# Performance work log

Hardware: AMD Instinct MI355X
Metric: run time of the kernel (lower is better)

## Reference

```python
import jax, jax.numpy as jnp
import numpy as np

B, L, D = 2, 2048, 1024
H, HD = 16, 64

def setup_inputs() -> dict:
    key = jax.random.key(0)
    ks = jax.random.split(key, 5)
    x = jax.random.normal(ks[0], (B, L, D), dtype=jnp.float32)
    mask = jnp.ones((B, L, L), dtype=bool)
    # torch nn.Linear weights: [out_features, in_features]
    s = 1.0 / np.sqrt(D)
    wq = jax.random.normal(ks[1], (H * HD, D), dtype=jnp.float32) * s
    wk = jax.random.normal(ks[2], (H * HD, D), dtype=jnp.float32) * s
    wv = jax.random.normal(ks[3], (H * HD, D), dtype=jnp.float32) * s
    wo = jax.random.normal(ks[4], (D, H * HD), dtype=jnp.float32) * s
    return {"x": x, "mask": mask, "wq": wq, "wk": wk, "wv": wv, "wo": wo}

def reference(x, mask, wq, wk, wv, wo):
    b, l, d = x.shape
    scale = jnp.sqrt(jnp.float32(HD))
    # projections (Linear: x @ W.T), then split heads -> [B,H,L,HD]
    q = (x @ wq.T).reshape(b, l, H, HD).transpose(0, 2, 1, 3)
    k = (x @ wk.T).reshape(b, l, H, HD).transpose(0, 2, 1, 3)
    v = (x @ wv.T).reshape(b, l, H, HD).transpose(0, 2, 1, 3)
    scores = jnp.einsum('bhqd,bhkd->bhqk', q, k) / scale
    scores = jnp.where(mask[:, None, :, :], scores, -jnp.inf)
    attn = jax.nn.softmax(scores, axis=-1)
    out = jnp.einsum('bhqk,bhkd->bhqd', attn, v)
    out = out.transpose(0, 2, 1, 3).reshape(b, l, H * HD)
    return out @ wo.T
```

## Files before the change

kernel.cpp:

```cpp
#include <hip/hip_runtime.h>
#include <hip/hip_bf16.h>

#define B_ 2
#define L_ 2048
#define D_ 1024
#define H_ 16
#define HD_ 64

typedef __bf16 bf16_t;
typedef bf16_t bf16x8 __attribute__((ext_vector_type(8)));
typedef bf16_t bf16x4 __attribute__((ext_vector_type(4)));
typedef float f32x2 __attribute__((ext_vector_type(2)));
typedef float f32x4 __attribute__((ext_vector_type(4)));
typedef float f32x16 __attribute__((ext_vector_type(16)));
typedef unsigned int u32x4 __attribute__((ext_vector_type(4)));

static __device__ __forceinline__ f32x4 mfma16(bf16x8 a, bf16x8 b, f32x4 c) {
    return __builtin_amdgcn_mfma_f32_16x16x32_bf16(a, b, c, 0, 0, 0);
}
static __device__ __forceinline__ f32x16 mfma32(bf16x8 a, bf16x8 b, f32x16 c) {
    return __builtin_amdgcn_mfma_f32_32x32x16_bf16(a, b, c, 0, 0, 0);
}
static __device__ __forceinline__ unsigned cvtpk(float a, float b) {
    unsigned r;
    asm("v_cvt_pk_bf16_f32 %0, %1, %2" : "=v"(r) : "v"(a), "v"(b));
    return r;
}

__global__ void cvt_all(const float* __restrict__ x,  const float* __restrict__ wq,
                        const float* __restrict__ wk, const float* __restrict__ wv,
                        const float* __restrict__ wo, bf16_t* __restrict__ dst) {
    const int NX = B_ * L_ * D_;
    const int NW = D_ * D_;
    int i = (blockIdx.x * blockDim.x + threadIdx.x) * 4;
    const float* s; int off;
    if      (i < NX)          { s = x;  off = i; }
    else if (i < NX + NW)     { s = wq; off = i - NX; }
    else if (i < NX + 2 * NW) { s = wk; off = i - NX - NW; }
    else if (i < NX + 3 * NW) { s = wv; off = i - NX - 2 * NW; }
    else                      { s = wo; off = i - NX - 3 * NW; }
    float4 v = *reinterpret_cast<const float4*>(s + off);
    bf16x4 o;
    o[0] = (bf16_t)v.x; o[1] = (bf16_t)v.y; o[2] = (bf16_t)v.z; o[3] = (bf16_t)v.w;
    *reinterpret_cast<bf16x4*>(dst + i) = o;
}

template<int MODE>
__global__ __launch_bounds__(256) void gemm_lds(const bf16_t* __restrict__ A,
                                                const bf16_t* __restrict__ Bt,
                                                void* __restrict__ Cout) {
    constexpr int K = 1024;
    __shared__ __align__(16) bf16_t lA[2][128][32];
    __shared__ __align__(16) bf16_t lB[2][128][32];
    const int tid = threadIdx.x, wave = tid >> 6, lane = tid & 63;
    const int lo = lane & 15, hi = lane >> 4;
    const int bm = blockIdx.x * 128, bn = blockIdx.y * 128;
    const int wm = (wave >> 1) * 64, wn = (wave & 1) * 64;
    const int srow = wave * 32 + (lane >> 2);
    const int skel = (lane & 3) * 8;

    const bf16_t* Abase = A  + (size_t)(bm + srow) * K + skel;
    const bf16_t* Bbase = Bt + (size_t)(bn + srow) * K + skel;

    auto stage = [&](int buf, int k0) {
#pragma unroll
        for (int t = 0; t < 2; ++t) {
            __builtin_amdgcn_global_load_lds(
                (const __attribute__((address_space(1))) void*)(Abase + (size_t)t * 16 * K + k0),
                (__attribute__((address_space(3))) void*)&lA[buf][wave * 32 + t * 16][0],
                16, 0, 0);
            __builtin_amdgcn_global_load_lds(
                (const __attribute__((address_space(1))) void*)(Bbase + (size_t)t * 16 * K + k0),
                (__attribute__((address_space(3))) void*)&lB[buf][wave * 32 + t * 16][0],
                16, 0, 0);
        }
    };

    f32x4 acc[4][4] = {};
    auto compute = [&](int buf) {
        bf16x8 af[4], bfr[4];
#pragma unroll
        for (int i = 0; i < 4; ++i)
            af[i] = *reinterpret_cast<const bf16x8*>(&lA[buf][wm + i * 16 + lo][hi * 8]);
#pragma unroll
        for (int j = 0; j < 4; ++j)
            bfr[j] = *reinterpret_cast<const bf16x8*>(&lB[buf][wn + j * 16 + lo][hi * 8]);
#pragma unroll
        for (int i = 0; i < 4; ++i)
#pragma unroll
            for (int j = 0; j < 4; ++j)
                acc[i][j] = mfma16(af[i], bfr[j], acc[i][j]);
    };

    stage(0, 0);
    __syncthreads();
#pragma unroll 1
    for (int k0 = 0; k0 < K; k0 += 64) {
        stage(1, k0 + 32);
        compute(0);
        __syncthreads();
        if (k0 + 64 < K) stage(0, k0 + 64);
        compute(1);
        __syncthreads();
    }

    const int region = bn >> 10;
#pragma unroll
    for (int i = 0; i < 4; ++i)
#pragma unroll
        for (int j = 0; j < 4; ++j)
#pragma unroll
            for (int r = 0; r < 4; ++r) {
                int m = bm + wm + i * 16 + hi * 4 + r;
                int n = bn + wn + j * 16 + lo;
                float v = acc[i][j][r];
                if constexpr (MODE == 1) {
                    reinterpret_cast<float*>(Cout)[(size_t)m * 1024 + n] = v;
                } else {
                    if (region == 0) v *= 0.18033688011113885f;
                    int nl = n & 1023;
                    int b = m >> 11, l = m & 2047;
                    int h = nl >> 6, hd = nl & 63;
                    size_t base = (size_t)region * 4194304 +
                                  ((size_t)(b * H_ + h)) * (L_ * HD_);
                    size_t idx;
                    if (region == 0) {
                        idx = base + (size_t)l * HD_ + hd;
                    } else if (region == 1) {
                        idx = base + (size_t)(l >> 6) * 4096 +
                              ((((l >> 5) & 1) * 4 + (hd >> 4)) * 64 +
                               ((hd >> 3) & 1) * 32 + (l & 31)) * 8 + (hd & 7);
                    } else {
                        idx = base + (size_t)(l >> 6) * 4096 +
                              (((hd >> 5) * 4 + ((l >> 4) & 3)) * 64 +
                               ((l >> 3) & 1) * 32 + (hd & 31)) * 8 + (l & 7);
                    }
                    reinterpret_cast<bf16_t*>(Cout)[idx] = (bf16_t)v;
                }
            }
}

template<int CHUNKS>
__global__ __launch_bounds__(256, 2) void fattn(const bf16_t* __restrict__ Q,
                                                const bf16_t* __restrict__ Kp,
                                                const bf16_t* __restrict__ Vp,
                                                bf16_t* __restrict__ Oout,
                                                bf16_t* __restrict__ Opart,
                                                float* __restrict__ Spart) {
    __shared__ __align__(16) bf16_t ldsK[2][4096];
    __shared__ __align__(16) bf16_t ldsV[2][4096];
    const int tid = threadIdx.x, wave = tid >> 6, lane = tid & 63;
    const int q5 = lane & 31, hp = lane >> 5;
    const int hh = blockIdx.y;
    const int b = blockIdx.z & (B_ - 1), chunk = blockIdx.z >> 1;
    constexpr int NT = (L_ / CHUNKS) / 64;
    const int t0 = chunk * NT;
    const bf16_t* Qh  = Q  + (size_t)(b * H_ + hh) * L_ * HD_;
    const bf16_t* Khp = Kp + (size_t)(b * H_ + hh) * L_ * HD_;
    const bf16_t* Vhp = Vp + (size_t)(b * H_ + hh) * L_ * HD_;
    const int qb = blockIdx.x * 128 + wave * 32;

    bf16x8 qf[4];
#pragma unroll
    for (int s = 0; s < 4; ++s)
        qf[s] = *reinterpret_cast<const bf16x8*>(
            Qh + (size_t)(qb + q5) * HD_ + s * 16 + hp * 8);

    f32x16 oacc[2] = {};
    f32x2 sr2 = {0.f, 0.f};

    auto stage = [&](int buf, int tg) {
        const bf16_t* gK = Khp + (size_t)tg * 4096 + wave * 512 + lane * 8;
        const bf16_t* gV = Vhp + (size_t)tg * 4096 + wave * 512 + lane * 8;
#pragma unroll
        for (int r = 0; r < 2; ++r) {
            __builtin_amdgcn_global_load_lds(
                (const __attribute__((address_space(1))) void*)(gK + r * 2048),
                (__attribute__((address_space(3))) void*)&ldsK[buf][r * 2048 + wave * 512],
                16, 0, 0);
            __builtin_amdgcn_global_load_lds(
                (const __attribute__((address_space(1))) void*)(gV + r * 2048),
                (__attribute__((address_space(3))) void*)&ldsV[buf][r * 2048 + wave * 512],
                16, 0, 0);
        }
    };

    stage(0, t0);
    __syncthreads();
#pragma unroll 1
    for (int ti = 0; ti < NT; ++ti) {
        const int buf = ti & 1;
        if (ti + 1 < NT) stage(buf ^ 1, t0 + ti + 1);

        bf16x8 kf[2][4];
#pragma unroll
        for (int kg = 0; kg < 2; ++kg)
#pragma unroll
            for (int s = 0; s < 4; ++s)
                kf[kg][s] = *reinterpret_cast<const bf16x8*>(
                    &ldsK[buf][(kg * 4 + s) * 512 + lane * 8]);

        f32x16 sT[2];
#pragma unroll
        for (int kg = 0; kg < 2; ++kg) {
            f32x16 z = {};
#pragma unroll
            for (int s = 0; s < 4; ++s) z = mfma32(kf[kg][s], qf[s], z);
            sT[kg] = z;
        }

        unsigned pw[2][8];
#pragma unroll
        for (int kg = 0; kg < 2; ++kg)
#pragma unroll
            for (int j = 0; j < 8; ++j) {
                float p0 = exp2f(sT[kg][2 * j]);
                float p1 = exp2f(sT[kg][2 * j + 1]);
                f32x2 pp = {p0, p1};
                sr2 += pp;
                pw[kg][j] = cvtpk(p0, p1);
            }

#pragma unroll
        for (int ks = 0; ks < 4; ++ks) {
            const int kg = ks >> 1, bb = (ks & 1) * 4;
            unsigned a0 = pw[kg][bb + 0], a1 = pw[kg][bb + 1];
            unsigned b0 = pw[kg][bb + 2], b1 = pw[kg][bb + 3];
            asm("v_permlane32_swap_b32 %0, %1" : "+v"(a0), "+v"(b0));
            asm("v_permlane32_swap_b32 %0, %1" : "+v"(a1), "+v"(b1));
            u32x4 w; w[0] = a0; w[1] = a1; w[2] = b0; w[3] = b1;
            bf16x8 pf = __builtin_bit_cast(bf16x8, w);
#pragma unroll
            for (int hdg = 0; hdg < 2; ++hdg) {
                bf16x8 vfr = *reinterpret_cast<const bf16x8*>(
                    &ldsV[buf][(hdg * 4 + ks) * 512 + lane * 8]);
                oacc[hdg] = mfma32(vfr, pf, oacc[hdg]);
            }
        }

        __syncthreads();
    }

    float srun = sr2[0] + sr2[1];
    float stot = srun + __shfl_xor(srun, 32);

    if constexpr (CHUNKS == 1) {
        float inv = 1.f / stot;
        const size_t obase = ((size_t)(b * L_ + qb + q5) * H_ + hh) * HD_;
#pragma unroll
        for (int hdg = 0; hdg < 2; ++hdg)
#pragma unroll
            for (int j = 0; j < 4; ++j) {
                bf16x4 o;
#pragma unroll
                for (int i = 0; i < 4; ++i)
                    o[i] = (bf16_t)(oacc[hdg][4 * j + i] * inv);
                *reinterpret_cast<bf16x4*>(Oout + obase + hdg * 32 + 8 * j + 4 * hp) = o;
            }
    } else {
        const size_t row = (size_t)(b * H_ + hh) * L_ + qb + q5;
        bf16_t* Ob = Opart + (size_t)chunk * (B_ * H_ * L_ * HD_) + row * HD_;
#pragma unroll
        for (int hdg = 0; hdg < 2; ++hdg)
#pragma unroll
            for (int j = 0; j < 4; ++j) {
                bf16x4 o;
#pragma unroll
                for (int i = 0; i < 4; ++i)
                    o[i] = (bf16_t)oacc[hdg][4 * j + i];
                *reinterpret_cast<bf16x4*>(Ob + hdg * 32 + 8 * j + 4 * hp) = o;
            }
        if (hp == 0) Spart[(size_t)chunk * (B_ * H_ * L_) + row] = stot;
    }
}

__global__ void combine(const bf16_t* __restrict__ Op, const float* __restrict__ Sp,
                        bf16_t* __restrict__ Ab) {
    const size_t PS = (size_t)B_ * H_ * L_ * HD_;
    int i = blockIdx.x * blockDim.x + threadIdx.x;
    int hd4 = (i & 15) * 4;
    int row = i >> 4;
    int l = row & (L_ - 1);
    int bh = row >> 11;
    int h = bh & (H_ - 1), b = bh >> 4;
    bf16x4 A0 = *reinterpret_cast<const bf16x4*>(Op + (size_t)row * HD_ + hd4);
    bf16x4 A1 = *reinterpret_cast<const bf16x4*>(Op + PS + (size_t)row * HD_ + hd4);
    float inv = 1.f / (Sp[row] + Sp[B_ * H_ * L_ + row]);
    bf16x4 o;
#pragma unroll
    for (int t = 0; t < 4; ++t)
        o[t] = (bf16_t)(((float)A0[t] + (float)A1[t]) * inv);
    size_t oi = ((size_t)(b * L_ + l) * H_ + h) * HD_ + hd4;
    *reinterpret_cast<bf16x4*>(Ab + oi) = o;
}

extern "C" void kernel_launch(void* const* d_in, const int* in_sizes, int n_in,
                              void* d_out, int out_size, void* d_ws, size_t ws_size,
                              hipStream_t stream) {
    const float* x  = (const float*)d_in[0];
    const float* wq = (const float*)d_in[2];
    const float* wk = (const float*)d_in[3];
    const float* wv = (const float*)d_in[4];
    const float* wo = (const float*)d_in[5];

    char* ws = (char*)d_ws;
    const size_t MB = 1024 * 1024;
    bf16_t* xb    = (bf16_t*)(ws);
    bf16_t* wqkvb = (bf16_t*)(ws + 8 * MB);
    bf16_t* wob   = (bf16_t*)(ws + 14 * MB);
    bf16_t* Qb    = (bf16_t*)(ws + 16 * MB);
    bf16_t* Kpb   = (bf16_t*)(ws + 24 * MB);
    bf16_t* Vpb   = (bf16_t*)(ws + 32 * MB);
    bf16_t* Ab    = (bf16_t*)(ws + 40 * MB);
    bf16_t* Opart = (bf16_t*)(ws + 48 * MB);
    float*  Spart = (float*)(ws + 66 * MB);

    cvt_all<<<8192, 256, 0, stream>>>(x, wq, wk, wv, wo, xb);

    gemm_lds<0><<<dim3(32, 24), 256, 0, stream>>>(xb, wqkvb, Qb);

    if (ws_size >= 83 * MB) {
        fattn<2><<<dim3(L_ / 128, H_, B_ * 2), 256, 0, stream>>>(
            Qb, Kpb, Vpb, Ab, Opart, Spart);
        combine<<<(B_ * H_ * L_ * 16) / 256, 256, 0, stream>>>(Opart, Spart, Ab);
    } else {
        fattn<1><<<dim3(L_ / 128, H_, B_), 256, 0, stream>>>(
            Qb, Kpb, Vpb, Ab, nullptr, nullptr);
    }

    gemm_lds<1><<<dim3(32, 8), 256, 0, stream>>>(Ab, wob, d_out);
}
```

Baseline: 133.5 us.

## Split attention into four KV chunks, remap blocks across XCDs, smaller-tile output GEMM

Attention now splits the KV sequence into four chunks instead of two, doubling the block count. The combine kernel is generalized to sum any number of partials, and Spart moves in the workspace to fit the larger partial buffer. Flat block IDs are remapped so consecutive work items spread across the eight XCDs, aiming for better cache locality per head. The output projection gets its own 64x128-tile GEMM, doubling its grid to fill more CUs, at the cost of extra partial-output traffic and less reuse per block.

```diff
diff --git a/kernel.cpp b/kernel.cpp
--- a/kernel.cpp
+++ b/kernel.cpp
@@ -45,10 +45,9 @@
     *reinterpret_cast<bf16x4*>(dst + i) = o;
 }
 
-template<int MODE>
-__global__ __launch_bounds__(256) void gemm_lds(const bf16_t* __restrict__ A,
+__global__ __launch_bounds__(256) void gemm_qkv(const bf16_t* __restrict__ A,
                                                 const bf16_t* __restrict__ Bt,
-                                                void* __restrict__ Cout) {
+                                                bf16_t* __restrict__ Cout) {
     constexpr int K = 1024;
     __shared__ __align__(16) bf16_t lA[2][128][32];
     __shared__ __align__(16) bf16_t lB[2][128][32];
@@ -114,29 +113,96 @@
                 int m = bm + wm + i * 16 + hi * 4 + r;
                 int n = bn + wn + j * 16 + lo;
                 float v = acc[i][j][r];
-                if constexpr (MODE == 1) {
-                    reinterpret_cast<float*>(Cout)[(size_t)m * 1024 + n] = v;
+                if (region == 0) v *= 0.18033688011113885f;
+                int nl = n & 1023;
+                int b = m >> 11, l = m & 2047;
+                int h = nl >> 6, hd = nl & 63;
+                size_t base = (size_t)region * 4194304 +
+                              ((size_t)(b * H_ + h)) * (L_ * HD_);
+                size_t idx;
+                if (region == 0) {
+                    idx = base + (size_t)l * HD_ + hd;
+                } else if (region == 1) {
+                    idx = base + (size_t)(l >> 6) * 4096 +
+                          ((((l >> 5) & 1) * 4 + (hd >> 4)) * 64 +
+                           ((hd >> 3) & 1) * 32 + (l & 31)) * 8 + (hd & 7);
                 } else {
-                    if (region == 0) v *= 0.18033688011113885f;
-                    int nl = n & 1023;
-                    int b = m >> 11, l = m & 2047;
-                    int h = nl >> 6, hd = nl & 63;
-                    size_t base = (size_t)region * 4194304 +
-                                  ((size_t)(b * H_ + h)) * (L_ * HD_);
-                    size_t idx;
-                    if (region == 0) {
-                        idx = base + (size_t)l * HD_ + hd;
-                    } else if (region == 1) {
-                        idx = base + (size_t)(l >> 6) * 4096 +
-                              ((((l >> 5) & 1) * 4 + (hd >> 4)) * 64 +
-                               ((hd >> 3) & 1) * 32 + (l & 31)) * 8 + (hd & 7);
-                    } else {
-                        idx = base + (size_t)(l >> 6) * 4096 +
-                              (((hd >> 5) * 4 + ((l >> 4) & 3)) * 64 +
-                               ((l >> 3) & 1) * 32 + (hd & 31)) * 8 + (l & 7);
-                    }
-                    reinterpret_cast<bf16_t*>(Cout)[idx] = (bf16_t)v;
+                    idx = base + (size_t)(l >> 6) * 4096 +
+                          (((hd >> 5) * 4 + ((l >> 4) & 3)) * 64 +
+                           ((l >> 3) & 1) * 32 + (hd & 31)) * 8 + (l & 7);
                 }
+                Cout[idx] = (bf16_t)v;
+            }
+}
+
+__global__ __launch_bounds__(256) void gemm_ao(const bf16_t* __restrict__ A,
+                                               const bf16_t* __restrict__ Bt,
+                                               float* __restrict__ Cout) {
+    constexpr int K = 1024;
+    __shared__ __align__(16) bf16_t lA[2][64][32];
+    __shared__ __align__(16) bf16_t lB[2][128][32];
+    const int tid = threadIdx.x, wave = tid >> 6, lane = tid & 63;
+    const int lo = lane & 15, hi = lane >> 4;
+    const int bm = blockIdx.x * 64, bn = blockIdx.y * 128;
+    const int wn = wave * 32;
+    const int srow = wave * 16 + (lane >> 2);
+    const int skel = (lane & 3) * 8;
+
+    const bf16_t* Abase = A  + (size_t)(bm + srow) * K + skel;
+    const bf16_t* Bbase = Bt + (size_t)(bn + srow) * K + skel;
+
+    auto stage = [&](int buf, int k0) {
+        __builtin_amdgcn_global_load_lds(
+            (const __attribute__((address_space(1))) void*)(Abase + k0),
+            (__attribute__((address_space(3))) void*)&lA[buf][wave * 16][0],
+            16, 0, 0);
+        __builtin_amdgcn_global_load_lds(
+            (const __attribute__((address_space(1))) void*)(Bbase + k0),
+            (__attribute__((address_space(3))) void*)&lB[buf][wave * 16][0],
+            16, 0, 0);
+        __builtin_amdgcn_global_load_lds(
+            (const __attribute__((address_space(1))) void*)(Bbase + (size_t)64 * K + k0),
+            (__attribute__((address_space(3))) void*)&lB[buf][64 + wave * 16][0],
+            16, 0, 0);
+    };
+
+    f32x4 acc[4][2] = {};
+    auto compute = [&](int buf) {
+        bf16x8 af[4], bfr[2];
+#pragma unroll
+        for (int i = 0; i < 4; ++i)
+            af[i] = *reinterpret_cast<const bf16x8*>(&lA[buf][i * 16 + lo][hi * 8]);
+#pragma unroll
+        for (int j = 0; j < 2; ++j)
+            bfr[j] = *reinterpret_cast<const bf16x8*>(&lB[buf][wn + j * 16 + lo][hi * 8]);
+#pragma unroll
+        for (int i = 0; i < 4; ++i)
+#pragma unroll
+            for (int j = 0; j < 2; ++j)
+                acc[i][j] = mfma16(af[i], bfr[j], acc[i][j]);
+    };
+
+    stage(0, 0);
+    __syncthreads();
+#pragma unroll 1
+    for (int k0 = 0; k0 < K; k0 += 64) {
+        stage(1, k0 + 32);
+        compute(0);
+        __syncthreads();
+        if (k0 + 64 < K) stage(0, k0 + 64);
+        compute(1);
+        __syncthreads();
+    }
+
+#pragma unroll
+    for (int i = 0; i < 4; ++i)
+#pragma unroll
+        for (int j = 0; j < 2; ++j)
+#pragma unroll
+            for (int r = 0; r < 4; ++r) {
+                int m = bm + i * 16 + hi * 4 + r;
+                int n = bn + wn + j * 16 + lo;
+                Cout[(size_t)m * 1024 + n] = acc[i][j][r];
             }
 }
 
@@ -151,14 +217,23 @@
     __shared__ __align__(16) bf16_t ldsV[2][4096];
     const int tid = threadIdx.x, wave = tid >> 6, lane = tid & 63;
     const int q5 = lane & 31, hp = lane >> 5;
-    const int hh = blockIdx.y;
-    const int b = blockIdx.z & (B_ - 1), chunk = blockIdx.z >> 1;
+
+    constexpr int TOTAL = (L_ / 128) * H_ * (B_ * CHUNKS);
+    constexpr int PER = TOTAL / 8;
+    const int bid = blockIdx.x + (L_ / 128) * (blockIdx.y + H_ * blockIdx.z);
+    const int wid = (bid & 7) * PER + (bid >> 3);
+    const int qx = wid & 15;
+    const int grp = wid >> 4;
+    const int hh = grp & (H_ - 1);
+    const int zz = grp >> 4;
+    const int b = zz & (B_ - 1), chunk = zz >> 1;
+
     constexpr int NT = (L_ / CHUNKS) / 64;
     const int t0 = chunk * NT;
     const bf16_t* Qh  = Q  + (size_t)(b * H_ + hh) * L_ * HD_;
     const bf16_t* Khp = Kp + (size_t)(b * H_ + hh) * L_ * HD_;
     const bf16_t* Vhp = Vp + (size_t)(b * H_ + hh) * L_ * HD_;
-    const int qb = blockIdx.x * 128 + wave * 32;
+    const int qb = qx * 128 + wave * 32;
 
     bf16x8 qf[4];
 #pragma unroll
@@ -274,6 +349,7 @@
     }
 }
 
+template<int CHUNKS>
 __global__ void combine(const bf16_t* __restrict__ Op, const float* __restrict__ Sp,
                         bf16_t* __restrict__ Ab) {
     const size_t PS = (size_t)B_ * H_ * L_ * HD_;
@@ -283,13 +359,20 @@
     int l = row & (L_ - 1);
     int bh = row >> 11;
     int h = bh & (H_ - 1), b = bh >> 4;
-    bf16x4 A0 = *reinterpret_cast<const bf16x4*>(Op + (size_t)row * HD_ + hd4);
-    bf16x4 A1 = *reinterpret_cast<const bf16x4*>(Op + PS + (size_t)row * HD_ + hd4);
-    float inv = 1.f / (Sp[row] + Sp[B_ * H_ * L_ + row]);
+    f32x4 acc = {};
+    float s = 0.f;
+#pragma unroll
+    for (int c = 0; c < CHUNKS; ++c) {
+        bf16x4 A = *reinterpret_cast<const bf16x4*>(
+            Op + (size_t)c * PS + (size_t)row * HD_ + hd4);
+#pragma unroll
+        for (int t = 0; t < 4; ++t) acc[t] += (float)A[t];
+        s += Sp[(size_t)c * (B_ * H_ * L_) + row];
+    }
+    float inv = 1.f / s;
     bf16x4 o;
 #pragma unroll
-    for (int t = 0; t < 4; ++t)
-        o[t] = (bf16_t)(((float)A0[t] + (float)A1[t]) * inv);
+    for (int t = 0; t < 4; ++t) o[t] = (bf16_t)(acc[t] * inv);
     size_t oi = ((size_t)(b * L_ + l) * H_ + h) * HD_ + hd4;
     *reinterpret_cast<bf16x4*>(Ab + oi) = o;
 }
@@ -313,20 +396,20 @@
     bf16_t* Vpb   = (bf16_t*)(ws + 32 * MB);
     bf16_t* Ab    = (bf16_t*)(ws + 40 * MB);
     bf16_t* Opart = (bf16_t*)(ws + 48 * MB);
-    float*  Spart = (float*)(ws + 66 * MB);
+    float*  Spart = (float*)(ws + 82 * MB);
 
     cvt_all<<<8192, 256, 0, stream>>>(x, wq, wk, wv, wo, xb);
 
-    gemm_lds<0><<<dim3(32, 24), 256, 0, stream>>>(xb, wqkvb, Qb);
+    gemm_qkv<<<dim3(32, 24), 256, 0, stream>>>(xb, wqkvb, Qb);
 
     if (ws_size >= 83 * MB) {
-        fattn<2><<<dim3(L_ / 128, H_, B_ * 2), 256, 0, stream>>>(
+        fattn<4><<<dim3(L_ / 128, H_, B_ * 4), 256, 0, stream>>>(
             Qb, Kpb, Vpb, Ab, Opart, Spart);
-        combine<<<(B_ * H_ * L_ * 16) / 256, 256, 0, stream>>>(Opart, Spart, Ab);
+        combine<4><<<(B_ * H_ * L_ * 16) / 256, 256, 0, stream>>>(Opart, Spart, Ab);
     } else {
         fattn<1><<<dim3(L_ / 128, H_, B_), 256, 0, stream>>>(
             Qb, Kpb, Vpb, Ab, nullptr, nullptr);
     }
 
-    gemm_lds<1><<<dim3(32, 8), 256, 0, stream>>>(Ab, wob, d_out);
-}
+    gemm_ao<<<dim3(64, 8), 256, 0, stream>>>(Ab, wob, (float*)d_out);
+}
```

Result: no change. 134.6 us (+0.8%).
